# Performance work log

Measured on AMD Instinct MI355X. Metric: run time of the kernel, lower is better.

## Reference

```python
import jax, jax.numpy as jnp
import numpy as np

EMB = 1024
HEADS = 16
HEAD_DIM = EMB // HEADS
HIDDEN = 4 * EMB
SEQ = 2048
BATCH = 4


def setup_inputs() -> dict:
    key = jax.random.key(0)
    ks = jax.random.split(key, 16)
    s = 0.02
    return {
        "x": jax.random.normal(ks[0], (BATCH, SEQ, EMB), jnp.float32),
        "ln1_scale": jnp.ones((EMB,), jnp.float32),
        "ln1_shift": jnp.zeros((EMB,), jnp.float32),
        "ln2_scale": jnp.ones((EMB,), jnp.float32),
        "ln2_shift": jnp.zeros((EMB,), jnp.float32),
        # weights stored [in, out]; y = x @ W + b (equivalent to torch Linear)
        "W_q": jax.random.normal(ks[1], (EMB, EMB), jnp.float32) * s,
        "W_k": jax.random.normal(ks[2], (EMB, EMB), jnp.float32) * s,
        "W_v": jax.random.normal(ks[3], (EMB, EMB), jnp.float32) * s,
        "W_o": jax.random.normal(ks[4], (EMB, EMB), jnp.float32) * s,
        "b_o": jnp.zeros((EMB,), jnp.float32),
        "W_fc": jax.random.normal(ks[5], (EMB, HIDDEN), jnp.float32) * s,
        "b_fc": jnp.zeros((HIDDEN,), jnp.float32),
        "W_proj": jax.random.normal(ks[6], (HIDDEN, EMB), jnp.float32) * s,
        "b_proj": jnp.zeros((EMB,), jnp.float32),
    }


def _layernorm(x, scale, shift, eps=1e-5):
    mean = jnp.mean(x, axis=-1, keepdims=True)
    var = jnp.mean(jnp.square(x - mean), axis=-1, keepdims=True)  # unbiased=False
    return scale * (x - mean) / jnp.sqrt(var + eps) + shift


def _gelu(x):
    c = jnp.sqrt(jnp.asarray(2.0 / jnp.pi, x.dtype))
    return 0.5 * x * (1.0 + jnp.tanh(c * (x + 0.044715 * x ** 3)))


def _attention(x, W_q, W_k, W_v, W_o, b_o):
    b, s, _ = x.shape
    q = (x @ W_q).reshape(b, s, HEADS, HEAD_DIM)
    k = (x @ W_k).reshape(b, s, HEADS, HEAD_DIM)
    v = (x @ W_v).reshape(b, s, HEADS, HEAD_DIM)
    scores = jnp.einsum("bqhd,bkhd->bhqk", q, k)
    causal = jnp.tril(jnp.ones((s, s), bool))  # keep lower-triangular
    scores = jnp.where(causal, scores, -jnp.inf)
    w = jax.nn.softmax(scores / jnp.sqrt(jnp.asarray(HEAD_DIM, x.dtype)), axis=-1)
    ctx = jnp.einsum("bhqk,bkhd->bqhd", w, v).reshape(b, s, EMB)
    return ctx @ W_o + b_o


def reference(x, ln1_scale, ln1_shift, ln2_scale, ln2_shift,
              W_q, W_k, W_v, W_o, b_o, W_fc, b_fc, W_proj, b_proj):
    h = x + _attention(_layernorm(x, ln1_scale, ln1_shift), W_q, W_k, W_v, W_o, b_o)
    m = _layernorm(h, ln2_scale, ln2_shift)
    m = _gelu(m @ W_fc + b_fc) @ W_proj + b_proj
    return h + m
```

## Files before the change

### kernel.cpp

```cpp
#include <hip/hip_runtime.h>

typedef __attribute__((ext_vector_type(8))) short bf16x8;
typedef __attribute__((ext_vector_type(2))) unsigned uint2v;
typedef __attribute__((ext_vector_type(4))) float f32x4;

#define MFMA_BF16(a, b, c) __builtin_amdgcn_mfma_f32_16x16x32_bf16((a), (b), (c), 0, 0, 0)
#define VMCNT(N) asm volatile("s_waitcnt vmcnt(" #N ")" ::: "memory")
#define BAR() asm volatile("s_barrier" ::: "memory")

__device__ __forceinline__ unsigned short bf16rn(float f) {
  unsigned u = __builtin_bit_cast(unsigned, f);
  u += 0x7fffu + ((u >> 16) & 1u);
  return (unsigned short)(u >> 16);
}

__device__ __forceinline__ void gld_lds16(const void* g, void* l) {
  __builtin_amdgcn_global_load_lds((const __attribute__((address_space(1))) void*)g,
                                   (__attribute__((address_space(3))) void*)l, 16, 0, 0);
}

__global__ __launch_bounds__(256) void convT_kernel(
    const float* __restrict__ wq, const float* __restrict__ wk,
    const float* __restrict__ wv, const float* __restrict__ wo,
    const float* __restrict__ wfc, const float* __restrict__ wpj,
    unsigned short* __restrict__ wsb)
{
  const int bid = blockIdx.x;
  const float* src; unsigned short* dst; int K, N, lb;
  if (bid < 1024) {
    const int m = bid >> 8; lb = bid & 255; K = 1024; N = 1024;
    src = (m == 0) ? wq : (m == 1) ? wk : (m == 2) ? wv : wo;
    dst = wsb + (size_t)m * 1048576u;
  } else if (bid < 2048) {
    lb = bid - 1024; K = 1024; N = 4096; src = wfc; dst = wsb + 4194304u;
  } else {
    lb = bid - 2048; K = 4096; N = 1024; src = wpj; dst = wsb + 8388608u;
  }
  const int tiles_k = K >> 6;
  const int tk = lb % tiles_k, tn = lb / tiles_k;
  const int k0 = tk << 6, n0 = tn << 6;
  const int t = threadIdx.x, kq = t & 15, nq = t >> 4;
  float4 r[4];
#pragma unroll
  for (int i = 0; i < 4; ++i)
    r[i] = *(const float4*)(src + (size_t)(k0 + kq * 4 + i) * N + n0 + nq * 4);
#pragma unroll
  for (int j = 0; j < 4; ++j) {
    ushort4 o;
    o.x = bf16rn(((const float*)&r[0])[j]);
    o.y = bf16rn(((const float*)&r[1])[j]);
    o.z = bf16rn(((const float*)&r[2])[j]);
    o.w = bf16rn(((const float*)&r[3])[j]);
    *(ushort4*)(dst + (size_t)(n0 + nq * 4 + j) * K + k0 + kq * 4) = o;
  }
}

__global__ __launch_bounds__(256) void ln_kernel(
    const float* __restrict__ x, const float* __restrict__ sc,
    const float* __restrict__ sh, unsigned short* __restrict__ out)
{
  const int row = blockIdx.x, t = threadIdx.x;
  const float4 v = *(const float4*)(x + (size_t)row * 1024 + t * 4);
  float s = v.x + v.y + v.z + v.w;
  float q = v.x * v.x + v.y * v.y + v.z * v.z + v.w * v.w;
#pragma unroll
  for (int off = 1; off < 64; off <<= 1) { s += __shfl_xor(s, off); q += __shfl_xor(q, off); }
  __shared__ float ps[4], pq[4];
  if ((t & 63) == 0) { ps[t >> 6] = s; pq[t >> 6] = q; }
  __syncthreads();
  s = ps[0] + ps[1] + ps[2] + ps[3];
  q = pq[0] + pq[1] + pq[2] + pq[3];
  const float mean = s * (1.f / 1024.f);
  const float var = q * (1.f / 1024.f) - mean * mean;
  const float inv = rsqrtf(var + 1e-5f);
  const float4 scv = *(const float4*)(sc + t * 4);
  const float4 shv = *(const float4*)(sh + t * 4);
  ushort4 o;
  o.x = bf16rn((v.x - mean) * inv * scv.x + shv.x);
  o.y = bf16rn((v.y - mean) * inv * scv.y + shv.y);
  o.z = bf16rn((v.z - mean) * inv * scv.z + shv.z);
  o.w = bf16rn((v.w - mean) * inv * scv.w + shv.w);
  *(ushort4*)(out + (size_t)row * 1024 + t * 4) = o;
}

template<int EPI>
__global__ __launch_bounds__(256, 2) void g128(
    const unsigned short* __restrict__ A, const unsigned short* __restrict__ Bt,
    int N, int K,
    unsigned short* __restrict__ outb, float* __restrict__ outf,
    const float* __restrict__ bias, const float* __restrict__ resid)
{
  extern __shared__ char smem[];
  constexpr int BUFSZ = 32768;
  const int t = threadIdx.x, lane = t & 63, w = t >> 6;
  const int g = lane >> 4, l15 = lane & 15;
  const int wr = w >> 1, wc = w & 1;
  const int bid = blockIdx.x;
  const int tm = (bid & 7) * 8 + ((bid >> 3) & 7);
  const int tn = bid >> 6;
  const int m0 = tm << 7, n0 = tn << 7;

  const int srow = t >> 3;
  const int colswz = (((t & 7) ^ (srow & 7)) << 3);
  const unsigned short* pA = A + (size_t)(m0 + srow) * K + colswz;
  const unsigned short* pB = Bt + (size_t)(n0 + srow) * K + colswz;
  const int ldw = w << 10;

  auto stA = [&](int TT, char* buf) {
#pragma unroll
    for (int i = 0; i < 4; ++i)
      gld_lds16(pA + TT * 64 + (size_t)(i * 32) * K, buf + i * 4096 + ldw);
  };
  auto stB02 = [&](int TT, char* buf) {
    gld_lds16(pB + TT * 64, buf + 16384 + ldw);
    gld_lds16(pB + TT * 64 + (size_t)64 * K, buf + 16384 + 8192 + ldw);
  };
  auto stB13 = [&](int TT, char* buf) {
    gld_lds16(pB + TT * 64 + (size_t)32 * K, buf + 16384 + 4096 + ldw);
    gld_lds16(pB + TT * 64 + (size_t)96 * K, buf + 16384 + 12288 + ldw);
  };

  const int sw0 = (((0 + g) ^ (l15 & 7)) << 4);
  const int sw1 = (((4 + g) ^ (l15 & 7)) << 4);
  const int NT = K >> 6;

  f32x4 acc[4][4] = {};
  bf16x8 av[4][2], bv0[2][2], bv1[2][2];

#define LDA_ALL(CB) { _Pragma("unroll") for (int mi = 0; mi < 4; ++mi) {                  \
    const int row_ = (wr * 64 + mi * 16 + l15) * 128;                                     \
    av[mi][0] = *(const bf16x8*)((CB) + row_ + sw0);                                      \
    av[mi][1] = *(const bf16x8*)((CB) + row_ + sw1); } }
#define LDB_H(CB, H, BV) { _Pragma("unroll") for (int ni = 0; ni < 2; ++ni) {             \
    const int row_ = 16384 + (wc * 64 + (H) * 32 + ni * 16 + l15) * 128;                  \
    BV[ni][0] = *(const bf16x8*)((CB) + row_ + sw0);                                      \
    BV[ni][1] = *(const bf16x8*)((CB) + row_ + sw1); } }
#define MMH(BV, H) { __builtin_amdgcn_s_setprio(1);                                       \
    _Pragma("unroll") for (int mi = 0; mi < 4; ++mi)                                      \
      _Pragma("unroll") for (int ni = 0; ni < 2; ++ni) {                                  \
        acc[mi][(H)*2+ni] = MFMA_BF16(av[mi][0], BV[ni][0], acc[mi][(H)*2+ni]);           \
        acc[mi][(H)*2+ni] = MFMA_BF16(av[mi][1], BV[ni][1], acc[mi][(H)*2+ni]);  }        \
    __builtin_amdgcn_s_setprio(0); }

  stA(0, smem); stB02(0, smem); stB13(0, smem);
  stA(1, smem + BUFSZ); stB02(1, smem + BUFSZ);
  VMCNT(6);
  BAR();

  for (int kt = 0; kt < NT; ++kt) {
    char* cb = smem + (kt & 1) * BUFSZ;
    char* ob = smem + ((kt & 1) ^ 1) * BUFSZ;
    LDA_ALL(cb);
    LDB_H(cb, 0, bv0);
    if (kt + 1 < NT) stB13(kt + 1, ob);
    BAR();
    MMH(bv0, 0);
    BAR();
    LDB_H(cb, 1, bv1);
    if (kt + 2 < NT) { stA(kt + 2, cb); stB02(kt + 2, cb); VMCNT(6); }
    else if (kt + 1 < NT) VMCNT(0);
    BAR();
    MMH(bv1, 1);
    BAR();
  }
#undef LDA_ALL
#undef LDB_H
#undef MMH

  if constexpr (EPI == 2) {
#pragma unroll
    for (int mi = 0; mi < 4; ++mi) {
      const int ro = mi * 16 + g * 4;
#pragma unroll
      for (int ci = 0; ci < 4; ++ci) {
        const int n = n0 + wc * 64 + ((ci >> 1) << 5) + ((ci & 1) << 4) + l15;
        const float bn = bias[n];
#pragma unroll
        for (int r = 0; r < 4; ++r) {
          const size_t m = m0 + wr * 64 + ro + r;
          outf[m * N + n] = acc[mi][ci][r] + bn + resid[m * N + n];
        }
      }
    }
  } else if constexpr (EPI == 1) {
    __syncthreads();
    unsigned short* T = (unsigned short*)(smem + w * 9216);
#pragma unroll
    for (int mi = 0; mi < 4; ++mi)
#pragma unroll
      for (int ci = 0; ci < 4; ++ci) {
        const int co = ((ci >> 1) << 5) + ((ci & 1) << 4);
#pragma unroll
        for (int r = 0; r < 4; ++r)
          T[(co + l15) * 72 + mi * 16 + 4 * g + r] = bf16rn(acc[mi][ci][r]);
      }
    asm volatile("s_waitcnt lgkmcnt(0)" ::: "memory");
    const int bidx = m0 >> 11;
    const int srw = (m0 & 2047) + wr * 64 + ((lane & 7) << 3);
#pragma unroll
    for (int rr = 0; rr < 8; ++rr) {
      const int trow = rr * 8 + (lane >> 3);
      bf16x8 v = *(const bf16x8*)((char*)T + trow * 144 + ((lane & 7) << 4));
      *(bf16x8*)(outb + (size_t)(bidx * 1024 + n0 + wc * 64 + trow) * 2048 + srw) = v;
    }
  } else {
    __syncthreads();
    char* wsl = smem + w * 8192;
#pragma unroll
    for (int mi = 0; mi < 4; ++mi) {
      const int ro = mi * 16 + g * 4;
#pragma unroll
      for (int ci = 0; ci < 4; ++ci) {
        const int co = ((ci >> 1) << 5) + ((ci & 1) << 4) + l15;
        float bn = 0.f;
        if constexpr (EPI == 3) bn = bias[n0 + wc * 64 + co];
#pragma unroll
        for (int r = 0; r < 4; ++r) {
          float v = acc[mi][ci][r];
          if constexpr (EPI == 3) {
            v += bn;
            const float inner = v + 0.044715f * v * v * v;
            const float s = exp2f(-2.3022085f * inner);
            v = v / (1.0f + s);
          }
          *(unsigned short*)(wsl + (ro + r) * 128 + ((co * 2 + g * 32) & 127)) = bf16rn(v);
        }
      }
    }
#pragma unroll
    for (int s = 0; s < 8; ++s) {
      const int row = s * 8 + (lane >> 3);
      bf16x8 vv = *(const bf16x8*)(wsl + row * 128 +
                                   (((lane & 7) * 16 + ((row >> 2) & 3) * 32) & 127));
      *(bf16x8*)(outb + (size_t)(m0 + wr * 64 + row) * N + n0 + wc * 64 + (lane & 7) * 8) = vv;
    }
  }
}

__global__ __launch_bounds__(512) void attn_kernel(
    const unsigned short* __restrict__ qg, const unsigned short* __restrict__ kg,
    const unsigned short* __restrict__ vT, unsigned short* __restrict__ ctx)
{
  __shared__ char smem[36864];
  const int bh = blockIdx.x, b = bh >> 4, h = bh & 15;
  const int t = threadIdx.x, lane = t & 63, w = t >> 6, g = lane >> 4, l15 = lane & 15;
  char* Ks = smem;
  char* Vs = smem + 8192;
  char* Pt = smem + 16384 + w * 2560;

  const float SC = 0.18033688011112042f;

  const int srow = t >> 3;
  const int ssw = ((((t & 7) << 4) ^ ((srow & 7) << 4)) >> 1);

  for (int pass = 0; pass < 2; ++pass) {
    const int qt = pass ? 15 - (int)blockIdx.y : (int)blockIdx.y;
    const int q0 = qt << 7;
    const int q0w = q0 + w * 16;

    bf16x8 qf[2];
#pragma unroll
    for (int ks = 0; ks < 2; ++ks)
      qf[ks] = *(const bf16x8*)(qg + (size_t)(b * 2048 + q0w + l15) * 2048 +
                                h * 64 + ks * 32 + g * 8);

    f32x4 acc[4] = {};
    float lsum[4] = {};

    const int ntile = 2 * qt + 2;
    for (int kt = 0; kt < ntile; ++kt) {
      const int kv0 = kt << 6;
      __syncthreads();
      gld_lds16(kg + (size_t)(b * 2048 + kv0 + srow) * 2048 + h * 64 + ssw,
                Ks + ((t >> 3) << 7));
      gld_lds16(vT + (size_t)(b * 1024 + h * 64 + srow) * 2048 + kv0 + ssw,
                Vs + ((t >> 3) << 7));
      __syncthreads();

      f32x4 sf[4] = {};
#pragma unroll
      for (int nb = 0; nb < 4; ++nb) {
        const int krow = nb * 16 + l15;
#pragma unroll
        for (int ks = 0; ks < 2; ++ks) {
          bf16x8 kf = *(const bf16x8*)(Ks + krow * 128 +
                                       (((ks * 32 + g * 8) << 1) ^ ((krow & 7) << 4)));
          sf[nb] = MFMA_BF16(qf[ks], kf, sf[nb]);
        }
      }
      if (kv0 + 63 > q0w) {
#pragma unroll
        for (int nb = 0; nb < 4; ++nb)
#pragma unroll
          for (int r = 0; r < 4; ++r) {
            const int qq = q0w + 4 * g + r;
            const int kk = kv0 + nb * 16 + l15;
            if (kk > qq) sf[nb][r] = -__builtin_inff();
          }
      }
#pragma unroll
      for (int nb = 0; nb < 4; ++nb)
#pragma unroll
        for (int r = 0; r < 4; ++r) {
          const float p = exp2f(__builtin_fmaf(sf[nb][r], SC, -4.0f));
          sf[nb][r] = p;
          lsum[r] += p;
        }
#pragma unroll
      for (int nb = 0; nb < 4; ++nb) {
        uint2v dw;
        asm("v_cvt_pk_bf16_f32 %0, %1, %2"
            : "=v"(dw.x) : "v"(sf[nb][0]), "v"(sf[nb][1]));
        asm("v_cvt_pk_bf16_f32 %0, %1, %2"
            : "=v"(dw.y) : "v"(sf[nb][2]), "v"(sf[nb][3]));
        *(uint2v*)(Pt + (nb * 16 + l15) * 40 + (g << 3)) = dw;
      }
      asm volatile("s_waitcnt lgkmcnt(0)" ::: "memory");
#pragma unroll
      for (int ks = 0; ks < 2; ++ks) {
        const char* pp = Pt + (ks * 32 + g * 8) * 40 + (l15 << 1);
        bf16x8 pa;
#pragma unroll
        for (int jj = 0; jj < 8; ++jj)
          pa[jj] = *(const short*)(pp + jj * 40);
#pragma unroll
        for (int nb = 0; nb < 4; ++nb) {
          const int drow = nb * 16 + l15;
          bf16x8 vb = *(const bf16x8*)(Vs + drow * 128 +
                                       (((ks * 32 + g * 8) << 1) ^ ((drow & 7) << 4)));
          acc[nb] = MFMA_BF16(pa, vb, acc[nb]);
        }
      }
    }
#pragma unroll
    for (int r = 0; r < 4; ++r) {
      float s = lsum[r];
      s += __shfl_xor(s, 1);
      s += __shfl_xor(s, 2);
      s += __shfl_xor(s, 4);
      s += __shfl_xor(s, 8);
      lsum[r] = s;
    }
    float inv[4];
#pragma unroll
    for (int r = 0; r < 4; ++r) inv[r] = 1.0f / lsum[r];
#pragma unroll
    for (int nb = 0; nb < 4; ++nb)
#pragma unroll
      for (int r = 0; r < 4; ++r)
        ctx[(size_t)(b * 2048 + q0w + 4 * g + r) * 1024 + h * 64 + nb * 16 + l15] =
            bf16rn(acc[nb][r] * inv[r]);
  }
}

extern "C" void kernel_launch(void* const* d_in, const int* in_sizes, int n_in,
                              void* d_out, int out_size, void* d_ws, size_t ws_size,
                              hipStream_t stream)
{
  const float* x   = (const float*)d_in[0];
  const float* l1s = (const float*)d_in[1];
  const float* l1b = (const float*)d_in[2];
  const float* l2s = (const float*)d_in[3];
  const float* l2b = (const float*)d_in[4];
  const float* Wq  = (const float*)d_in[5];
  const float* Wk  = (const float*)d_in[6];
  const float* Wv  = (const float*)d_in[7];
  const float* Wo  = (const float*)d_in[8];
  const float* bo  = (const float*)d_in[9];
  const float* Wfc = (const float*)d_in[10];
  const float* bfc = (const float*)d_in[11];
  const float* Wpj = (const float*)d_in[12];
  const float* bpj = (const float*)d_in[13];
  float* out = (float*)d_out;
  char* ws = (char*)d_ws;

  unsigned short* wT   = (unsigned short*)ws;
  unsigned short* wqkT = wT;
  unsigned short* wvT  = wT + 2097152u;
  unsigned short* woT  = wT + 3145728u;
  unsigned short* wfcT = wT + 4194304u;
  unsigned short* wpjT = wT + 8388608u;
  unsigned short* ln1x = (unsigned short*)(ws + 25165824u);
  unsigned short* qkb  = (unsigned short*)(ws + 41943040u);
  unsigned short* vTb  = (unsigned short*)(ws + 75497472u);
  unsigned short* ctx  = (unsigned short*)(ws + 92274688u);
  unsigned short* ln2x = ctx;
  float* hbuf          = (float*)(ws + 109051904u);
  unsigned short* fcb  = (unsigned short*)(ws + 25165824u);

  convT_kernel<<<3072, 256, 0, stream>>>(Wq, Wk, Wv, Wo, Wfc, Wpj, wT);
  ln_kernel<<<8192, 256, 0, stream>>>(x, l1s, l1b, ln1x);
  g128<0><<<1024, 256, 65536, stream>>>(ln1x, wqkT, 2048, 1024,
                                        qkb, nullptr, nullptr, nullptr);
  g128<1><<<512, 256, 65536, stream>>>(ln1x, wvT, 1024, 1024,
                                       vTb, nullptr, nullptr, nullptr);
  attn_kernel<<<dim3(64, 8), 512, 0, stream>>>(qkb, qkb + 1024, vTb, ctx);
  g128<2><<<512, 256, 65536, stream>>>(ctx, woT, 1024, 1024,
                                       nullptr, hbuf, bo, x);
  ln_kernel<<<8192, 256, 0, stream>>>(hbuf, l2s, l2b, ln2x);
  g128<3><<<2048, 256, 65536, stream>>>(ln2x, wfcT, 4096, 1024,
                                        fcb, nullptr, bfc, nullptr);
  g128<2><<<512, 256, 65536, stream>>>(fcb, wpjT, 1024, 4096,
                                       nullptr, out, bpj, hbuf);
}
```

Measured before the change: 338.1 us.

## Single-buffer the A tile in GEMM to cut LDS and raise occupancy

The GEMM's A operand goes from double-buffered to a single LDS buffer, while B stays double-buffered, so LDS per block drops from 64KB to 48KB. Launch bounds are raised to 3 blocks per CU. The next A tile is now loaded only after all waves have read the current one into registers, which shortens the prefetch distance for A and may expose global load latency. The aim is to hide latency with more resident blocks rather than deeper per-block buffering.

```diff
diff --git a/kernel.cpp b/kernel.cpp
--- a/kernel.cpp
+++ b/kernel.cpp
@@ -84,14 +84,13 @@
 }
 
 template<int EPI>
-__global__ __launch_bounds__(256, 2) void g128(
+__global__ __launch_bounds__(256, 3) void g128(
     const unsigned short* __restrict__ A, const unsigned short* __restrict__ Bt,
     int N, int K,
     unsigned short* __restrict__ outb, float* __restrict__ outf,
     const float* __restrict__ bias, const float* __restrict__ resid)
 {
   extern __shared__ char smem[];
-  constexpr int BUFSZ = 32768;
   const int t = threadIdx.x, lane = t & 63, w = t >> 6;
   const int g = lane >> 4, l15 = lane & 15;
   const int wr = w >> 1, wc = w & 1;
@@ -106,18 +105,18 @@
   const unsigned short* pB = Bt + (size_t)(n0 + srow) * K + colswz;
   const int ldw = w << 10;
 
-  auto stA = [&](int TT, char* buf) {
+  auto stA = [&](int TT) {
 #pragma unroll
     for (int i = 0; i < 4; ++i)
-      gld_lds16(pA + TT * 64 + (size_t)(i * 32) * K, buf + i * 4096 + ldw);
+      gld_lds16(pA + TT * 64 + (size_t)(i * 32) * K, smem + i * 4096 + ldw);
   };
   auto stB02 = [&](int TT, char* buf) {
-    gld_lds16(pB + TT * 64, buf + 16384 + ldw);
-    gld_lds16(pB + TT * 64 + (size_t)64 * K, buf + 16384 + 8192 + ldw);
+    gld_lds16(pB + TT * 64, buf + ldw);
+    gld_lds16(pB + TT * 64 + (size_t)64 * K, buf + 8192 + ldw);
   };
   auto stB13 = [&](int TT, char* buf) {
-    gld_lds16(pB + TT * 64 + (size_t)32 * K, buf + 16384 + 4096 + ldw);
-    gld_lds16(pB + TT * 64 + (size_t)96 * K, buf + 16384 + 12288 + ldw);
+    gld_lds16(pB + TT * 64 + (size_t)32 * K, buf + 4096 + ldw);
+    gld_lds16(pB + TT * 64 + (size_t)96 * K, buf + 12288 + ldw);
   };
 
   const int sw0 = (((0 + g) ^ (l15 & 7)) << 4);
@@ -127,12 +126,12 @@
   f32x4 acc[4][4] = {};
   bf16x8 av[4][2], bv0[2][2], bv1[2][2];
 
-#define LDA_ALL(CB) { _Pragma("unroll") for (int mi = 0; mi < 4; ++mi) {                  \
+#define LDA_ALL() { _Pragma("unroll") for (int mi = 0; mi < 4; ++mi) {                    \
     const int row_ = (wr * 64 + mi * 16 + l15) * 128;                                     \
-    av[mi][0] = *(const bf16x8*)((CB) + row_ + sw0);                                      \
-    av[mi][1] = *(const bf16x8*)((CB) + row_ + sw1); } }
+    av[mi][0] = *(const bf16x8*)(smem + row_ + sw0);                                      \
+    av[mi][1] = *(const bf16x8*)(smem + row_ + sw1); } }
 #define LDB_H(CB, H, BV) { _Pragma("unroll") for (int ni = 0; ni < 2; ++ni) {             \
-    const int row_ = 16384 + (wc * 64 + (H) * 32 + ni * 16 + l15) * 128;                  \
+    const int row_ = (wc * 64 + (H) * 32 + ni * 16 + l15) * 128;                          \
     BV[ni][0] = *(const bf16x8*)((CB) + row_ + sw0);                                      \
     BV[ni][1] = *(const bf16x8*)((CB) + row_ + sw1); } }
 #define MMH(BV, H) { __builtin_amdgcn_s_setprio(1);                                       \
@@ -142,25 +141,27 @@
         acc[mi][(H)*2+ni] = MFMA_BF16(av[mi][1], BV[ni][1], acc[mi][(H)*2+ni]);  }        \
     __builtin_amdgcn_s_setprio(0); }
 
-  stA(0, smem); stB02(0, smem); stB13(0, smem);
-  stA(1, smem + BUFSZ); stB02(1, smem + BUFSZ);
-  VMCNT(6);
+  stA(0); stB02(0, smem + 16384); stB13(0, smem + 16384);
+  stB02(1, smem + 32768);
+  VMCNT(2);
   BAR();
 
   for (int kt = 0; kt < NT; ++kt) {
-    char* cb = smem + (kt & 1) * BUFSZ;
-    char* ob = smem + ((kt & 1) ^ 1) * BUFSZ;
-    LDA_ALL(cb);
-    LDB_H(cb, 0, bv0);
-    if (kt + 1 < NT) stB13(kt + 1, ob);
+    char* bc = smem + 16384 + (kt & 1) * 16384;
+    char* bn = smem + 16384 + ((kt & 1) ^ 1) * 16384;
+    LDA_ALL();
+    LDB_H(bc, 0, bv0);
+    if (kt + 1 < NT) stB13(kt + 1, bn);
     BAR();
     MMH(bv0, 0);
     BAR();
-    LDB_H(cb, 1, bv1);
-    if (kt + 2 < NT) { stA(kt + 2, cb); stB02(kt + 2, cb); VMCNT(6); }
-    else if (kt + 1 < NT) VMCNT(0);
+    LDB_H(bc, 1, bv1);
+    if (kt + 1 < NT) stA(kt + 1);
+    if (kt + 2 < NT) stB02(kt + 2, bc);
     BAR();
     MMH(bv1, 1);
+    if (kt + 2 < NT) VMCNT(2);
+    else if (kt + 1 < NT) VMCNT(0);
     BAR();
   }
 #undef LDA_ALL
@@ -390,16 +391,16 @@
 
   convT_kernel<<<3072, 256, 0, stream>>>(Wq, Wk, Wv, Wo, Wfc, Wpj, wT);
   ln_kernel<<<8192, 256, 0, stream>>>(x, l1s, l1b, ln1x);
-  g128<0><<<1024, 256, 65536, stream>>>(ln1x, wqkT, 2048, 1024,
+  g128<0><<<1024, 256, 49152, stream>>>(ln1x, wqkT, 2048, 1024,
                                         qkb, nullptr, nullptr, nullptr);
-  g128<1><<<512, 256, 65536, stream>>>(ln1x, wvT, 1024, 1024,
+  g128<1><<<512, 256, 49152, stream>>>(ln1x, wvT, 1024, 1024,
                                        vTb, nullptr, nullptr, nullptr);
   attn_kernel<<<dim3(64, 8), 512, 0, stream>>>(qkb, qkb + 1024, vTb, ctx);
-  g128<2><<<512, 256, 65536, stream>>>(ctx, woT, 1024, 1024,
+  g128<2><<<512, 256, 49152, stream>>>(ctx, woT, 1024, 1024,
                                        nullptr, hbuf, bo, x);
   ln_kernel<<<8192, 256, 0, stream>>>(hbuf, l2s, l2b, ln2x);
-  g128<3><<<2048, 256, 65536, stream>>>(ln2x, wfcT, 4096, 1024,
+  g128<3><<<2048, 256, 49152, stream>>>(ln2x, wfcT, 4096, 1024,
                                         fcb, nullptr, bfc, nullptr);
-  g128<2><<<512, 256, 65536, stream>>>(fcb, wpjT, 1024, 4096,
+  g128<2><<<512, 256, 49152, stream>>>(fcb, wpjT, 1024, 4096,
                                        nullptr, out, bpj, hbuf);
 }
```

Result: no change. 342.1 us (+1.2%).
